# Optimization experiments

Measured on AMD Instinct MI355X. Metric: run time of the kernel, lower is better.

The kernel has to match this reference:

```python
import jax, jax.numpy as jnp
import numpy as np

N = 8
IN_F = 64
OUT_F = 64
BATCH = 16
SEQ = 8192


def setup_inputs() -> dict:
    key = jax.random.key(0)
    k_x, k_a, k_s = jax.random.split(key, 3)
    x = jax.random.normal(k_x, (BATCH, SEQ, IN_F, N), dtype=jnp.float32)
    A = jax.random.normal(k_a, (N, N, N), dtype=jnp.float32) * 0.1
    # xavier_normal_ on view(n*out_features, in_features): std = sqrt(2/(fan_in+fan_out))
    std = float(np.sqrt(2.0 / (IN_F + N * OUT_F)))
    S = jax.random.normal(k_s, (N, OUT_F, IN_F), dtype=jnp.float32) * std
    bias = jnp.zeros((OUT_F * N,), dtype=jnp.float32)
    return {"x": x, "A": A, "S": S, "bias": bias}


def reference(x, A, S, bias):
    n = N
    out_f, in_f = S.shape[1], S.shape[2]
    batch_shape = x.shape[:-2]
    # H[a,b,c,d] = sum_i A[i,a,c] * S[i,b,d]; reshape rows=(a,b), cols=(c,d)
    H = jnp.einsum('iac,ibd->abcd', A, S).reshape(n * out_f, n * in_f)
    x_flat = x.reshape(*batch_shape, in_f * n)
    out_flat = x_flat @ H.T + bias  # [..., n*out_f]
    return out_flat.reshape(*batch_shape, out_f, n)
```

## Files before the change

### kernel.cpp

```cpp
#include <hip/hip_runtime.h>
#include <hip/hip_bf16.h>


#define MDIM (16 * 8192)
#define KD 512
#define ND 512
#define BM 128
#define BN 128
#define BK 32

typedef __attribute__((ext_vector_type(8))) short short8;
typedef __attribute__((ext_vector_type(4))) float f32x4;

__device__ __forceinline__ unsigned pack2_bf16(float x, float y) {
    union { __hip_bfloat162 h; unsigned u; } cv;
    cv.h = __float22bfloat162_rn(make_float2(x, y));
    return cv.u;
}

__device__ __forceinline__ short8 cvt_frag(f32x4 a, f32x4 b) {
    union { unsigned u[4]; short8 s; } r;
    r.u[0] = pack2_bf16(a.x, a.y);
    r.u[1] = pack2_bf16(a.z, a.w);
    r.u[2] = pack2_bf16(b.x, b.y);
    r.u[3] = pack2_bf16(b.z, b.w);
    return r.s;
}

__device__ __forceinline__ void async16(const void* g, void* l) {
    __builtin_amdgcn_global_load_lds(
        (const __attribute__((address_space(1))) unsigned*)g,
        (__attribute__((address_space(3))) unsigned*)l, 16, 0, 0);
}

__global__ void build_h(const float* __restrict__ A, const float* __restrict__ S,
                        __hip_bfloat16* __restrict__ H) {
    int idx = blockIdx.x * 256 + threadIdx.x;
    int j = idx >> 9, k = idx & 511;
    int a = j >> 6, b = j & 63, c = k >> 6, d = k & 63;
    float acc = 0.f;
#pragma unroll
    for (int i = 0; i < 8; ++i)
        acc += A[i * 64 + a * 8 + c] * S[i * 4096 + b * 64 + d];
    H[idx] = __float2bfloat16(acc);
}

__global__ __launch_bounds__(256)
void phm_gemm(const float* __restrict__ X, const __hip_bfloat16* __restrict__ Hm,
              const float* __restrict__ bias, float* __restrict__ out) {
    __shared__ float As[BM * BK];
    __shared__ __hip_bfloat16 Bs[BN * BK];

    const int tid = threadIdx.x;
    const int m0 = blockIdx.y * BM;
    const int n0 = blockIdx.x * BN;

    const float* ag[4]; void* al[4];
#pragma unroll
    for (int q = 0; q < 4; ++q) {
        int seg = q * 256 + tid;
        int row = seg >> 3;
        int c16 = (seg & 7) ^ (row & 7);
        ag[q] = X + (size_t)(m0 + row) * KD + c16 * 4;
        al[q] = (char*)As + seg * 16;
    }
    const __hip_bfloat16* bg[2]; void* bl[2];
#pragma unroll
    for (int q = 0; q < 2; ++q) {
        int seg = q * 256 + tid;
        int row = seg >> 2;
        int c16 = seg & 3;
        bg[q] = Hm + (size_t)(n0 + row) * KD + c16 * 8;
        bl[q] = (char*)Bs + seg * 16;
    }

    const int wave = tid >> 6, lane = tid & 63;
    const int wm = (wave >> 1) * 64, wn = (wave & 1) * 64;
    const int fr = lane & 15;
    const int fs = lane >> 4;
    const int ca = (2 * fs) ^ (fr & 7);
    const int cb = ca ^ 1;

    f32x4 acc[4][4];
#pragma unroll
    for (int i = 0; i < 4; ++i)
#pragma unroll
        for (int j = 0; j < 4; ++j) acc[i][j] = (f32x4)(0.f);

    for (int kt = 0; kt < KD / BK; ++kt) {
#pragma unroll
        for (int q = 0; q < 4; ++q) async16(ag[q] + kt * BK, al[q]);
#pragma unroll
        for (int q = 0; q < 2; ++q) async16(bg[q] + kt * BK, bl[q]);
        __syncthreads();

        short8 bfr[4];
#pragma unroll
        for (int ni = 0; ni < 4; ++ni)
            bfr[ni] = *(const short8*)(Bs + (wn + ni * 16 + fr) * BK + fs * 8);

#pragma unroll
        for (int mi = 0; mi < 4; ++mi) {
            const float* rp = As + (wm + mi * 16 + fr) * BK;
            f32x4 a0 = *(const f32x4*)(rp + ca * 4);
            f32x4 a1 = *(const f32x4*)(rp + cb * 4);
            short8 afr = cvt_frag(a0, a1);
#pragma unroll
            for (int ni = 0; ni < 4; ++ni)
                acc[mi][ni] = __builtin_amdgcn_mfma_f32_16x16x32_bf16(
                    afr, bfr[ni], acc[mi][ni], 0, 0, 0);
        }
        __syncthreads();
    }

    const int cm = wm + fs * 4;
    const int cn0 = n0 + wn + fr;
#pragma unroll
    for (int mi = 0; mi < 4; ++mi) {
#pragma unroll
        for (int ni = 0; ni < 4; ++ni) {
            int col = cn0 + ni * 16;
            float bv = bias[col];
            float* op = out + (size_t)(m0 + cm + mi * 16) * ND + col;
#pragma unroll
            for (int r = 0; r < 4; ++r)
                op[(size_t)r * ND] = acc[mi][ni][r] + bv;
        }
    }
}

extern "C" void kernel_launch(void* const* d_in, const int* in_sizes, int n_in,
                              void* d_out, int out_size, void* d_ws, size_t ws_size,
                              hipStream_t stream) {
    const float* x    = (const float*)d_in[0];
    const float* A    = (const float*)d_in[1];
    const float* S    = (const float*)d_in[2];
    const float* bias = (const float*)d_in[3];
    float* out = (float*)d_out;
    __hip_bfloat16* H = (__hip_bfloat16*)d_ws;

    build_h<<<dim3(512 * 512 / 256), dim3(256), 0, stream>>>(A, S, H);
    phm_gemm<<<dim3(ND / BN, MDIM / BM), dim3(256), 0, stream>>>(x, H, bias, out);
}
```

Baseline: 517.9 us.

## Drop LDS staging; each block computes all 512 columns from register-direct global loads

Replaces the 128x128 LDS-tiled GEMM with a 64-row block of 8 waves that together cover all 512 output columns. Each block reads its X rows once instead of once per column tile. X and H fragments are loaded straight from global memory into registers, with no shared memory or barriers. The trade-off is that every block re-reads the whole bf16 H matrix through the caches, and there is no explicit prefetch to hide load latency beyond a 2x unroll.

```diff
diff --git a/kernel.cpp b/kernel.cpp
--- a/kernel.cpp
+++ b/kernel.cpp
@@ -5,9 +5,7 @@
 #define MDIM (16 * 8192)
 #define KD 512
 #define ND 512
-#define BM 128
-#define BN 128
-#define BK 32
+#define BM 64
 
 typedef __attribute__((ext_vector_type(8))) short short8;
 typedef __attribute__((ext_vector_type(4))) float f32x4;
@@ -27,12 +25,6 @@
     return r.s;
 }
 
-__device__ __forceinline__ void async16(const void* g, void* l) {
-    __builtin_amdgcn_global_load_lds(
-        (const __attribute__((address_space(1))) unsigned*)g,
-        (__attribute__((address_space(3))) unsigned*)l, 16, 0, 0);
-}
-
 __global__ void build_h(const float* __restrict__ A, const float* __restrict__ S,
                         __hip_bfloat16* __restrict__ H) {
     int idx = blockIdx.x * 256 + threadIdx.x;
@@ -45,83 +37,61 @@
     H[idx] = __float2bfloat16(acc);
 }
 
-__global__ __launch_bounds__(256)
+__global__ __launch_bounds__(512)
 void phm_gemm(const float* __restrict__ X, const __hip_bfloat16* __restrict__ Hm,
               const float* __restrict__ bias, float* __restrict__ out) {
-    __shared__ float As[BM * BK];
-    __shared__ __hip_bfloat16 Bs[BN * BK];
-
     const int tid = threadIdx.x;
-    const int m0 = blockIdx.y * BM;
-    const int n0 = blockIdx.x * BN;
-
-    const float* ag[4]; void* al[4];
-#pragma unroll
-    for (int q = 0; q < 4; ++q) {
-        int seg = q * 256 + tid;
-        int row = seg >> 3;
-        int c16 = (seg & 7) ^ (row & 7);
-        ag[q] = X + (size_t)(m0 + row) * KD + c16 * 4;
-        al[q] = (char*)As + seg * 16;
-    }
-    const __hip_bfloat16* bg[2]; void* bl[2];
-#pragma unroll
-    for (int q = 0; q < 2; ++q) {
-        int seg = q * 256 + tid;
-        int row = seg >> 2;
-        int c16 = seg & 3;
-        bg[q] = Hm + (size_t)(n0 + row) * KD + c16 * 8;
-        bl[q] = (char*)Bs + seg * 16;
-    }
-
     const int wave = tid >> 6, lane = tid & 63;
-    const int wm = (wave >> 1) * 64, wn = (wave & 1) * 64;
+    const int wm = (wave >> 2) * 32;
+    const int wn = (wave & 3) * 128;
     const int fr = lane & 15;
     const int fs = lane >> 4;
-    const int ca = (2 * fs) ^ (fr & 7);
-    const int cb = ca ^ 1;
+    const size_t m0 = (size_t)blockIdx.x * BM;
 
-    f32x4 acc[4][4];
+    const float* ap0 = X + (m0 + wm + fr) * (size_t)KD + fs * 8;
+    const float* ap1 = ap0 + (size_t)16 * KD;
+    const __hip_bfloat16* bp[8];
 #pragma unroll
-    for (int i = 0; i < 4; ++i)
+    for (int ni = 0; ni < 8; ++ni)
+        bp[ni] = Hm + (size_t)(wn + ni * 16 + fr) * KD + fs * 8;
+
+    f32x4 acc[2][8];
 #pragma unroll
-        for (int j = 0; j < 4; ++j) acc[i][j] = (f32x4)(0.f);
+    for (int i = 0; i < 2; ++i)
+#pragma unroll
+        for (int j = 0; j < 8; ++j) acc[i][j] = (f32x4)(0.f);
 
-    for (int kt = 0; kt < KD / BK; ++kt) {
+#pragma unroll 2
+    for (int kt = 0; kt < KD / 32; ++kt) {
+        const int ko = kt * 32;
+        f32x4 a00 = *(const f32x4*)(ap0 + ko);
+        f32x4 a01 = *(const f32x4*)(ap0 + ko + 4);
+        f32x4 a10 = *(const f32x4*)(ap1 + ko);
+        f32x4 a11 = *(const f32x4*)(ap1 + ko + 4);
+        short8 bfr[8];
 #pragma unroll
-        for (int q = 0; q < 4; ++q) async16(ag[q] + kt * BK, al[q]);
+        for (int ni = 0; ni < 8; ++ni)
+            bfr[ni] = *(const short8*)(bp[ni] + ko);
+        short8 af0 = cvt_frag(a00, a01);
+        short8 af1 = cvt_frag(a10, a11);
 #pragma unroll
-        for (int q = 0; q < 2; ++q) async16(bg[q] + kt * BK, bl[q]);
-        __syncthreads();
-
-        short8 bfr[4];
+        for (int ni = 0; ni < 8; ++ni)
+            acc[0][ni] = __builtin_amdgcn_mfma_f32_16x16x32_bf16(
+                af0, bfr[ni], acc[0][ni], 0, 0, 0);
 #pragma unroll
-        for (int ni = 0; ni < 4; ++ni)
-            bfr[ni] = *(const short8*)(Bs + (wn + ni * 16 + fr) * BK + fs * 8);
-
-#pragma unroll
-        for (int mi = 0; mi < 4; ++mi) {
-            const float* rp = As + (wm + mi * 16 + fr) * BK;
-            f32x4 a0 = *(const f32x4*)(rp + ca * 4);
-            f32x4 a1 = *(const f32x4*)(rp + cb * 4);
-            short8 afr = cvt_frag(a0, a1);
-#pragma unroll
-            for (int ni = 0; ni < 4; ++ni)
-                acc[mi][ni] = __builtin_amdgcn_mfma_f32_16x16x32_bf16(
-                    afr, bfr[ni], acc[mi][ni], 0, 0, 0);
-        }
-        __syncthreads();
+        for (int ni = 0; ni < 8; ++ni)
+            acc[1][ni] = __builtin_amdgcn_mfma_f32_16x16x32_bf16(
+                af1, bfr[ni], acc[1][ni], 0, 0, 0);
     }
 
     const int cm = wm + fs * 4;
-    const int cn0 = n0 + wn + fr;
 #pragma unroll
-    for (int mi = 0; mi < 4; ++mi) {
+    for (int mi = 0; mi < 2; ++mi) {
 #pragma unroll
-        for (int ni = 0; ni < 4; ++ni) {
-            int col = cn0 + ni * 16;
+        for (int ni = 0; ni < 8; ++ni) {
+            int col = wn + ni * 16 + fr;
             float bv = bias[col];
-            float* op = out + (size_t)(m0 + cm + mi * 16) * ND + col;
+            float* op = out + (m0 + cm + mi * 16) * (size_t)ND + col;
 #pragma unroll
             for (int r = 0; r < 4; ++r)
                 op[(size_t)r * ND] = acc[mi][ni][r] + bv;
@@ -140,5 +110,5 @@
     __hip_bfloat16* H = (__hip_bfloat16*)d_ws;
 
     build_h<<<dim3(512 * 512 / 256), dim3(256), 0, stream>>>(A, S, H);
-    phm_gemm<<<dim3(ND / BN, MDIM / BM), dim3(256), 0, stream>>>(x, H, bias, out);
+    phm_gemm<<<dim3(MDIM / BM), dim3(512), 0, stream>>>(x, H, bias, out);
 }
```

Measured after the change: 706.2 us. 1.36x slower.
